# Kernel optimization log

Measured on AMD Instinct MI355X. Metric: run time of the kernel, lower is better.

## Reference

```python
import jax, jax.numpy as jnp
import numpy as np

NEG_INF = -jnp.inf


def setup_inputs() -> dict:
    key = jax.random.key(0)
    kq, kk, kv = jax.random.split(key, 3)
    B, L, H, E = 2, 2048, 16, 64
    queries = jax.random.normal(kq, (B, L, H, E), dtype=jnp.float32)
    keys = jax.random.normal(kk, (B, L, H, E), dtype=jnp.float32)
    values = jax.random.normal(kv, (B, L, H, E), dtype=jnp.float32)
    return {"queries": queries, "keys": keys, "values": values}


def reference(queries, keys, values):
    B, L, H, E = queries.shape
    scale = 1.0 / jnp.sqrt(jnp.asarray(E, dtype=queries.dtype))
    # scores: [B, H, L, S]
    scores = jnp.einsum("blhe,bshe->bhls", queries, keys)
    # causal mask: True above the diagonal -> masked out
    causal = jnp.triu(jnp.ones((L, L), dtype=bool), k=1)
    scores = jnp.where(causal[None, None, :, :], NEG_INF, scores)
    A = jax.nn.softmax(scale * scores, axis=-1)
    # output: [B, L, H, D]
    V = jnp.einsum("bhls,bshd->blhd", A, values)
    return V
```

## Files before the change

### kernel.cpp

```cpp
#include <hip/hip_runtime.h>


using f32x4  = __attribute__((ext_vector_type(4))) float;
using bf16x8 = __attribute__((ext_vector_type(8))) short;
using u32x2  = __attribute__((ext_vector_type(2))) unsigned int;
using u32x4  = __attribute__((ext_vector_type(4))) unsigned int;

constexpr int L = 2048;
constexpr int H = 16;
constexpr int E = 64;
constexpr int QBLK = 64;
constexpr int KVBLK = 64;
constexpr float QSC = 0.125f * 1.44269504088896f;
constexpr float THR = 8.0f;

__device__ __forceinline__ unsigned cvt_pk(float lo, float hi) {
    unsigned r;
    asm("v_cvt_pk_bf16_f32 %0, %1, %2" : "=v"(r) : "v"(lo), "v"(hi));
    return r;
}
__device__ __forceinline__ void pl16(unsigned& a, unsigned& b) {
    asm("v_permlane16_swap_b32 %0, %1" : "+v"(a), "+v"(b));
}
__device__ __forceinline__ void pl32(unsigned& a, unsigned& b) {
    asm("v_permlane32_swap_b32 %0, %1" : "+v"(a), "+v"(b));
}
__device__ __forceinline__ unsigned opaque_copy(unsigned a) {
    unsigned b;
    asm("v_mov_b32 %0, %1" : "=v"(b) : "v"(a));
    return b;
}
__device__ __forceinline__ float gmax4(float x) {
    unsigned a = __float_as_uint(x), b = opaque_copy(a);
    pl16(a, b);
    float m = fmaxf(__uint_as_float(a), __uint_as_float(b));
    unsigned c = __float_as_uint(m), d = opaque_copy(c);
    pl32(c, d);
    return fmaxf(__uint_as_float(c), __uint_as_float(d));
}
__device__ __forceinline__ float gsum4(float x) {
    unsigned a = __float_as_uint(x), b = opaque_copy(a);
    pl16(a, b);
    float s = __uint_as_float(a) + __uint_as_float(b);
    unsigned c = __float_as_uint(s), d = opaque_copy(c);
    pl32(c, d);
    return __uint_as_float(c) + __uint_as_float(d);
}
__device__ __forceinline__ int swz(int row, int bcol) {
    return (row * 128 + bcol) ^ ((row & 7) << 4);
}
__device__ __forceinline__ int swzV(int row, int bcol) {
    return (row * 128 + bcol) ^ ((((row & 7) ^ (row >> 3)) & 7) << 4);
}

__global__ __launch_bounds__(256, 4)
void fattn_kernel(const float* __restrict__ Q,
                  const float* __restrict__ K,
                  const float* __restrict__ V,
                  float* __restrict__ O)
{
    __shared__ short Kl[2][KVBLK * 64];
    __shared__ short Vl[2][64 * KVBLK];

    const int bx  = blockIdx.x;
    const int xcd = bx & 7;
    const int j   = bx >> 3;
    const int bh  = (j & 3) * 8 + xcd;
    const int v_  = j >> 2;
    const int q2  = v_ >> 3, x_ = v_ & 7;
    const int iq  = (q2 & 1) ? (31 - (q2 >> 1) - 2 * x_) : (2 * x_ + (q2 >> 1));
    const int h   = bh & 15;
    const int b   = bh >> 4;
    const int tid = threadIdx.x;
    const int w    = tid >> 6;
    const int lane = tid & 63;
    const int l16  = lane & 15;
    const int lhi  = lane >> 4;

    const size_t bhoff = (size_t)b * L * (H * E) + (size_t)h * E;
    const int rs_ = H * E;

    const int sv0 = (tid >> 4) * 4;
    const int d0  = (tid & 15) * 4;
    const int kc  = ((sv0 >> 3) & 1) * 32 + (sv0 >> 4) * 8 + (sv0 & 7);

    f32x4 ka[2][2];
    f32x4 va[4];

    auto issue_loads = [&](int t) {
        const int sb = t * KVBLK;
        #pragma unroll
        for (int g = 0; g < 2; ++g) {
            const int c = g * 256 + tid;
            const int s = c >> 3;
            const int e0 = (c & 7) * 8;
            const f32x4* kp = (const f32x4*)(K + bhoff + (size_t)(sb + s) * rs_ + e0);
            ka[g][0] = kp[0];
            ka[g][1] = kp[1];
        }
        #pragma unroll
        for (int jj = 0; jj < 4; ++jj)
            va[jj] = *(const f32x4*)(V + bhoff + (size_t)(sb + sv0 + jj) * rs_ + d0);
    };
    auto write_lds = [&](int bufi) {
        short* Kb = Kl[bufi];
        short* Vb = Vl[bufi];
        #pragma unroll
        for (int g = 0; g < 2; ++g) {
            const int c = g * 256 + tid;
            const int s = c >> 3;
            const int e0 = (c & 7) * 8;
            u32x4 kt;
            kt[0] = cvt_pk(ka[g][0][0], ka[g][0][1]);
            kt[1] = cvt_pk(ka[g][0][2], ka[g][0][3]);
            kt[2] = cvt_pk(ka[g][1][0], ka[g][1][1]);
            kt[3] = cvt_pk(ka[g][1][2], ka[g][1][3]);
            *(u32x4*)((char*)Kb + swz(s, e0 * 2)) = kt;
        }
        #pragma unroll
        for (int dd = 0; dd < 4; ++dd) {
            u32x2 vt;
            vt[0] = cvt_pk(va[0][dd], va[1][dd]);
            vt[1] = cvt_pk(va[2][dd], va[3][dd]);
            *(u32x2*)((char*)Vb + swzV(d0 + dd, kc * 2)) = vt;
        }
    };

    const int qg = iq * QBLK + w * 16 + l16;
    bf16x8 qf[2];
    {
        const float* qp = Q + bhoff + (size_t)qg * rs_ + lhi * 8;
        #pragma unroll
        for (int kf = 0; kf < 2; ++kf) {
            f32x4 xv = *(const f32x4*)(qp + kf * 32);
            f32x4 yv = *(const f32x4*)(qp + kf * 32 + 4);
            union { u32x4 u; bf16x8 hh; } r;
            r.u[0] = cvt_pk(xv[0] * QSC, xv[1] * QSC);
            r.u[1] = cvt_pk(xv[2] * QSC, xv[3] * QSC);
            r.u[2] = cvt_pk(yv[0] * QSC, yv[1] * QSC);
            r.u[3] = cvt_pk(yv[2] * QSC, yv[3] * QSC);
            qf[kf] = r.hh;
        }
    }

    float m_run = -INFINITY, lsum = 0.0f;
    f32x4 oacc[4];
    #pragma unroll
    for (int dt = 0; dt < 4; ++dt) oacc[dt] = (f32x4){0.f, 0.f, 0.f, 0.f};

    const int total = iq + 1;
    issue_loads(0);
    write_lds(0);
    if (total > 1) issue_loads(1);
    __syncthreads();

    for (int i = 0; i < total; ++i) {
        const char* Kb = (const char*)Kl[i & 1];
        const char* Vb = (const char*)Vl[i & 1];

        f32x4 p[4];
        #pragma unroll
        for (int st = 0; st < 4; ++st) p[st] = (f32x4){0.f, 0.f, 0.f, 0.f};
        __builtin_amdgcn_s_setprio(1);
        #pragma unroll
        for (int st = 0; st < 4; ++st) {
            #pragma unroll
            for (int kf = 0; kf < 2; ++kf) {
                bf16x8 af = *(const bf16x8*)(Kb + swz(st * 16 + l16, (lhi * 8 + kf * 32) * 2));
                p[st] = __builtin_amdgcn_mfma_f32_16x16x32_bf16(af, qf[kf], p[st], 0, 0, 0);
            }
        }
        __builtin_amdgcn_s_setprio(0);

        if (i == total - 1) {
            #pragma unroll
            for (int st = 0; st < 4; ++st)
                #pragma unroll
                for (int r = 0; r < 4; ++r) {
                    const int kg = i * KVBLK + st * 16 + lhi * 4 + r;
                    if (kg > qg) p[st][r] = -INFINITY;
                }
        }

        if (i + 1 < total) write_lds((i + 1) & 1);
        if (i + 2 < total) issue_loads(i + 2);

        float mx = -INFINITY;
        #pragma unroll
        for (int st = 0; st < 4; ++st)
            #pragma unroll
            for (int r = 0; r < 4; ++r) mx = fmaxf(mx, p[st][r]);
        mx = gmax4(mx);
        if (!__all(mx <= m_run + THR)) {
            const float mn = fmaxf(m_run, mx);
            const float corr = exp2f(m_run - mn);
            lsum *= corr;
            #pragma unroll
            for (int dt = 0; dt < 4; ++dt)
                #pragma unroll
                for (int r = 0; r < 4; ++r) oacc[dt][r] *= corr;
            m_run = mn;
        }
        float rsum = 0.f;
        #pragma unroll
        for (int st = 0; st < 4; ++st)
            #pragma unroll
            for (int r = 0; r < 4; ++r) {
                const float e = exp2f(p[st][r] - m_run);
                p[st][r] = e;
                rsum += e;
            }
        lsum += gsum4(rsum);

        unsigned wp[4][2];
        #pragma unroll
        for (int st = 0; st < 4; ++st) {
            wp[st][0] = cvt_pk(p[st][0], p[st][1]);
            wp[st][1] = cvt_pk(p[st][2], p[st][3]);
        }
        #pragma unroll
        for (int hh = 0; hh < 2; ++hh) {
            pl16(wp[0][hh], wp[1][hh]);
            pl16(wp[2][hh], wp[3][hh]);
            pl32(wp[0][hh], wp[2][hh]);
            pl32(wp[1][hh], wp[3][hh]);
        }
        union { u32x4 u; bf16x8 v; } pb0, pb1;
        pb0.u[0] = wp[0][0]; pb0.u[1] = wp[0][1];
        pb0.u[2] = wp[1][0]; pb0.u[3] = wp[1][1];
        pb1.u[0] = wp[2][0]; pb1.u[1] = wp[2][1];
        pb1.u[2] = wp[3][0]; pb1.u[3] = wp[3][1];

        __builtin_amdgcn_s_setprio(1);
        #pragma unroll
        for (int dt = 0; dt < 4; ++dt) {
            bf16x8 vf0 = *(const bf16x8*)(Vb + swzV(dt * 16 + l16, (lhi * 8) * 2));
            oacc[dt] = __builtin_amdgcn_mfma_f32_16x16x32_bf16(vf0, pb0.v, oacc[dt], 0, 0, 0);
            bf16x8 vf1 = *(const bf16x8*)(Vb + swzV(dt * 16 + l16, (lhi * 8 + 32) * 2));
            oacc[dt] = __builtin_amdgcn_mfma_f32_16x16x32_bf16(vf1, pb1.v, oacc[dt], 0, 0, 0);
        }
        __builtin_amdgcn_s_setprio(0);

        if (i + 1 < total) __syncthreads();
    }

    const float inv = 1.0f / lsum;
    float* op = O + bhoff + (size_t)qg * rs_;
    #pragma unroll
    for (int dt = 0; dt < 4; ++dt) {
        f32x4 o = oacc[dt];
        o[0] *= inv; o[1] *= inv; o[2] *= inv; o[3] *= inv;
        *(f32x4*)(op + dt * 16 + lhi * 4) = o;
    }
}

extern "C" void kernel_launch(void* const* d_in, const int* in_sizes, int n_in,
                              void* d_out, int out_size, void* d_ws, size_t ws_size,
                              hipStream_t stream) {
    const float* Q = (const float*)d_in[0];
    const float* K = (const float*)d_in[1];
    const float* V = (const float*)d_in[2];
    float* O = (float*)d_out;
    dim3 grid(1024);
    dim3 block(256);
    fattn_kernel<<<grid, block, 0, stream>>>(Q, K, V, O);
}
```

Baseline: 57.16 us.

## Pre-convert K/V to swizzled bf16 tiles in a prep kernel before attention

Adds a prep kernel that converts K and V to bf16 once, writing them into the workspace already in the swizzled LDS tile layout, with V transposed. The main attention kernel then copies these tiles straight from global memory into LDS, with no per-block fp32 loads, conversions or transposes. This removes the conversion work that every query block repeated for the same K/V tiles and halves the bytes each block reads. The cost is an extra kernel launch and a workspace round trip. The exp2 call is also switched to the hardware builtin, and the row max and row sum reductions are split into parallel chains.

Result: faster. 50.47 us (-11.7%).

```diff
diff --git a/kernel.cpp b/kernel.cpp
--- a/kernel.cpp
+++ b/kernel.cpp
@@ -14,6 +14,21 @@
 constexpr float QSC = 0.125f * 1.44269504088896f;
 constexpr float THR = 8.0f;
 
+#if defined(__has_builtin)
+#if __has_builtin(__builtin_amdgcn_exp2f)
+#define HAVE_EXP2 1
+#endif
+#endif
+__device__ __forceinline__ float fexp2(float x) {
+#ifdef HAVE_EXP2
+    return __builtin_amdgcn_exp2f(x);
+#else
+    float r;
+    asm("v_exp_f32 %0, %1" : "=v"(r) : "v"(x));
+    return r;
+#endif
+}
+
 __device__ __forceinline__ unsigned cvt_pk(float lo, float hi) {
     unsigned r;
     asm("v_cvt_pk_bf16_f32 %0, %1, %2" : "=v"(r) : "v"(lo), "v"(hi));
@@ -53,14 +68,64 @@
     return (row * 128 + bcol) ^ ((((row & 7) ^ (row >> 3)) & 7) << 4);
 }
 
+__global__ __launch_bounds__(256)
+void prep_kernel(const float* __restrict__ K, const float* __restrict__ V,
+                 short* __restrict__ Kb, short* __restrict__ Vb)
+{
+    __shared__ float Vt[64][65];
+    const int bx  = blockIdx.x;
+    const int t   = bx & 31;
+    const int bh  = bx >> 5;
+    const int tid = threadIdx.x;
+    const size_t bhoff = (size_t)(bh >> 4) * L * (H * E) + (size_t)(bh & 15) * E;
+    const size_t tileo = (size_t)(bh * 32 + t) * 4096;
+
+    #pragma unroll
+    for (int g = 0; g < 2; ++g) {
+        const int c  = g * 256 + tid;
+        const int r  = c >> 3;
+        const int e0 = (c & 7) * 8;
+        const float* kp = K + bhoff + (size_t)(t * 64 + r) * 1024 + e0;
+        f32x4 k0 = *(const f32x4*)kp, k1 = *(const f32x4*)(kp + 4);
+        u32x4 kt;
+        kt[0] = cvt_pk(k0[0], k0[1]); kt[1] = cvt_pk(k0[2], k0[3]);
+        kt[2] = cvt_pk(k1[0], k1[1]); kt[3] = cvt_pk(k1[2], k1[3]);
+        *(u32x4*)(Kb + tileo + r * 64 + (((e0 >> 3) ^ (r & 7)) * 8)) = kt;
+        const float* vp = V + bhoff + (size_t)(t * 64 + r) * 1024 + e0;
+        f32x4 v0 = *(const f32x4*)vp, v1 = *(const f32x4*)(vp + 4);
+        #pragma unroll
+        for (int k2 = 0; k2 < 4; ++k2) { Vt[r][e0 + k2] = v0[k2]; Vt[r][e0 + 4 + k2] = v1[k2]; }
+    }
+    __syncthreads();
+    #pragma unroll
+    for (int g = 0; g < 2; ++g) {
+        const int c  = g * 256 + tid;
+        const int d  = c >> 3;
+        const int jp = c & 7;
+        const int F  = ((d & 7) ^ (d >> 3)) & 7;
+        const int col0 = 8 * (jp ^ F);
+        float vals[8];
+        #pragma unroll
+        for (int i = 0; i < 8; ++i) {
+            const int col = col0 + i;
+            const int s = 16 * ((col >> 3) & 3) + 8 * (col >> 5) + (col & 7);
+            vals[i] = Vt[s][d];
+        }
+        u32x4 vt;
+        vt[0] = cvt_pk(vals[0], vals[1]); vt[1] = cvt_pk(vals[2], vals[3]);
+        vt[2] = cvt_pk(vals[4], vals[5]); vt[3] = cvt_pk(vals[6], vals[7]);
+        *(u32x4*)(Vb + tileo + d * 64 + jp * 8) = vt;
+    }
+}
+
 __global__ __launch_bounds__(256, 4)
-void fattn_kernel(const float* __restrict__ Q,
-                  const float* __restrict__ K,
-                  const float* __restrict__ V,
-                  float* __restrict__ O)
+void fattn_main(const float* __restrict__ Q,
+                const short* __restrict__ Kb,
+                const short* __restrict__ Vb,
+                float* __restrict__ O)
 {
-    __shared__ short Kl[2][KVBLK * 64];
-    __shared__ short Vl[2][64 * KVBLK];
+    __shared__ short Kl[2][4096];
+    __shared__ short Vl[2][4096];
 
     const int bx  = blockIdx.x;
     const int xcd = bx & 7;
@@ -69,24 +134,193 @@
     const int v_  = j >> 2;
     const int q2  = v_ >> 3, x_ = v_ & 7;
     const int iq  = (q2 & 1) ? (31 - (q2 >> 1) - 2 * x_) : (2 * x_ + (q2 >> 1));
-    const int h   = bh & 15;
-    const int b   = bh >> 4;
     const int tid = threadIdx.x;
     const int w    = tid >> 6;
     const int lane = tid & 63;
     const int l16  = lane & 15;
     const int lhi  = lane >> 4;
 
-    const size_t bhoff = (size_t)b * L * (H * E) + (size_t)h * E;
+    const size_t bhoff  = (size_t)(bh >> 4) * L * (H * E) + (size_t)(bh & 15) * E;
     const int rs_ = H * E;
-
+    const size_t kvbase = (size_t)bh * 32 * 4096;
+
+    u32x4 kreg[2], vreg[2];
+    auto stage_regs = [&](int t) {
+        const u32x4* kp = (const u32x4*)(Kb + kvbase + (size_t)t * 4096);
+        const u32x4* vp = (const u32x4*)(Vb + kvbase + (size_t)t * 4096);
+        #pragma unroll
+        for (int g = 0; g < 2; ++g) {
+            kreg[g] = kp[g * 256 + tid];
+            vreg[g] = vp[g * 256 + tid];
+        }
+    };
+    auto write_stage = [&](int buf) {
+        #pragma unroll
+        for (int g = 0; g < 2; ++g) {
+            ((u32x4*)Kl[buf])[g * 256 + tid] = kreg[g];
+            ((u32x4*)Vl[buf])[g * 256 + tid] = vreg[g];
+        }
+    };
+
+    const int qg = iq * QBLK + w * 16 + l16;
+    bf16x8 qf[2];
+    {
+        const float* qp = Q + bhoff + (size_t)qg * rs_ + lhi * 8;
+        #pragma unroll
+        for (int kf = 0; kf < 2; ++kf) {
+            f32x4 xv = *(const f32x4*)(qp + kf * 32);
+            f32x4 yv = *(const f32x4*)(qp + kf * 32 + 4);
+            union { u32x4 u; bf16x8 hh; } r;
+            r.u[0] = cvt_pk(xv[0] * QSC, xv[1] * QSC);
+            r.u[1] = cvt_pk(xv[2] * QSC, xv[3] * QSC);
+            r.u[2] = cvt_pk(yv[0] * QSC, yv[1] * QSC);
+            r.u[3] = cvt_pk(yv[2] * QSC, yv[3] * QSC);
+            qf[kf] = r.hh;
+        }
+    }
+
+    float m_run = -INFINITY, lsum = 0.0f;
+    f32x4 oacc[4];
+    #pragma unroll
+    for (int dt = 0; dt < 4; ++dt) oacc[dt] = (f32x4){0.f, 0.f, 0.f, 0.f};
+
+    const int total = iq + 1;
+    stage_regs(0);
+    write_stage(0);
+    if (total > 1) stage_regs(1);
+    __syncthreads();
+
+    for (int i = 0; i < total; ++i) {
+        const char* Kbl = (const char*)Kl[i & 1];
+        const char* Vbl = (const char*)Vl[i & 1];
+
+        f32x4 p[4];
+        #pragma unroll
+        for (int st = 0; st < 4; ++st) p[st] = (f32x4){0.f, 0.f, 0.f, 0.f};
+        __builtin_amdgcn_s_setprio(1);
+        #pragma unroll
+        for (int st = 0; st < 4; ++st) {
+            #pragma unroll
+            for (int kf = 0; kf < 2; ++kf) {
+                bf16x8 af = *(const bf16x8*)(Kbl + swz(st * 16 + l16, (lhi * 8 + kf * 32) * 2));
+                p[st] = __builtin_amdgcn_mfma_f32_16x16x32_bf16(af, qf[kf], p[st], 0, 0, 0);
+            }
+        }
+        __builtin_amdgcn_s_setprio(0);
+
+        if (i == total - 1) {
+            #pragma unroll
+            for (int st = 0; st < 4; ++st)
+                #pragma unroll
+                for (int r = 0; r < 4; ++r) {
+                    const int kg = i * KVBLK + st * 16 + lhi * 4 + r;
+                    if (kg > qg) p[st][r] = -INFINITY;
+                }
+        }
+
+        if (i + 1 < total) write_stage((i + 1) & 1);
+        if (i + 2 < total) stage_regs(i + 2);
+
+        f32x4 mv = p[0];
+        #pragma unroll
+        for (int st = 1; st < 4; ++st)
+            #pragma unroll
+            for (int r = 0; r < 4; ++r) mv[r] = fmaxf(mv[r], p[st][r]);
+        float mx = fmaxf(fmaxf(mv[0], mv[1]), fmaxf(mv[2], mv[3]));
+        mx = gmax4(mx);
+        if (!__all(mx <= m_run + THR)) {
+            const float mn = fmaxf(m_run, mx);
+            const float corr = fexp2(m_run - mn);
+            lsum *= corr;
+            #pragma unroll
+            for (int dt = 0; dt < 4; ++dt)
+                #pragma unroll
+                for (int r = 0; r < 4; ++r) oacc[dt][r] *= corr;
+            m_run = mn;
+        }
+        f32x4 rsv = (f32x4){0.f, 0.f, 0.f, 0.f};
+        #pragma unroll
+        for (int st = 0; st < 4; ++st)
+            #pragma unroll
+            for (int r = 0; r < 4; ++r) {
+                const float e = fexp2(p[st][r] - m_run);
+                p[st][r] = e;
+                rsv[r] += e;
+            }
+        lsum += gsum4((rsv[0] + rsv[1]) + (rsv[2] + rsv[3]));
+
+        unsigned wp[4][2];
+        #pragma unroll
+        for (int st = 0; st < 4; ++st) {
+            wp[st][0] = cvt_pk(p[st][0], p[st][1]);
+            wp[st][1] = cvt_pk(p[st][2], p[st][3]);
+        }
+        #pragma unroll
+        for (int hh = 0; hh < 2; ++hh) {
+            pl16(wp[0][hh], wp[1][hh]);
+            pl16(wp[2][hh], wp[3][hh]);
+            pl32(wp[0][hh], wp[2][hh]);
+            pl32(wp[1][hh], wp[3][hh]);
+        }
+        union { u32x4 u; bf16x8 v; } pb0, pb1;
+        pb0.u[0] = wp[0][0]; pb0.u[1] = wp[0][1];
+        pb0.u[2] = wp[1][0]; pb0.u[3] = wp[1][1];
+        pb1.u[0] = wp[2][0]; pb1.u[1] = wp[2][1];
+        pb1.u[2] = wp[3][0]; pb1.u[3] = wp[3][1];
+
+        __builtin_amdgcn_s_setprio(1);
+        #pragma unroll
+        for (int dt = 0; dt < 4; ++dt) {
+            bf16x8 vf0 = *(const bf16x8*)(Vbl + swzV(dt * 16 + l16, (lhi * 8) * 2));
+            oacc[dt] = __builtin_amdgcn_mfma_f32_16x16x32_bf16(vf0, pb0.v, oacc[dt], 0, 0, 0);
+            bf16x8 vf1 = *(const bf16x8*)(Vbl + swzV(dt * 16 + l16, (lhi * 8 + 32) * 2));
+            oacc[dt] = __builtin_amdgcn_mfma_f32_16x16x32_bf16(vf1, pb1.v, oacc[dt], 0, 0, 0);
+        }
+        __builtin_amdgcn_s_setprio(0);
+
+        if (i + 1 < total) __syncthreads();
+    }
+
+    const float inv = 1.0f / lsum;
+    float* op = O + bhoff + (size_t)qg * rs_;
+    #pragma unroll
+    for (int dt = 0; dt < 4; ++dt) {
+        f32x4 o = oacc[dt];
+        o[0] *= inv; o[1] *= inv; o[2] *= inv; o[3] *= inv;
+        *(f32x4*)(op + dt * 16 + lhi * 4) = o;
+    }
+}
+
+__global__ __launch_bounds__(256, 4)
+void fattn_fb(const float* __restrict__ Q,
+              const float* __restrict__ K,
+              const float* __restrict__ V,
+              float* __restrict__ O)
+{
+    __shared__ short Kl[2][KVBLK * 64];
+    __shared__ short Vl[2][64 * KVBLK];
+
+    const int bx  = blockIdx.x;
+    const int xcd = bx & 7;
+    const int j   = bx >> 3;
+    const int bh  = (j & 3) * 8 + xcd;
+    const int v_  = j >> 2;
+    const int q2  = v_ >> 3, x_ = v_ & 7;
+    const int iq  = (q2 & 1) ? (31 - (q2 >> 1) - 2 * x_) : (2 * x_ + (q2 >> 1));
+    const int tid = threadIdx.x;
+    const int w    = tid >> 6;
+    const int lane = tid & 63;
+    const int l16  = lane & 15;
+    const int lhi  = lane >> 4;
+
+    const size_t bhoff = (size_t)(bh >> 4) * L * (H * E) + (size_t)(bh & 15) * E;
+    const int rs_ = H * E;
     const int sv0 = (tid >> 4) * 4;
     const int d0  = (tid & 15) * 4;
     const int kc  = ((sv0 >> 3) & 1) * 32 + (sv0 >> 4) * 8 + (sv0 & 7);
 
     f32x4 ka[2][2];
     f32x4 va[4];
-
     auto issue_loads = [&](int t) {
         const int sb = t * KVBLK;
         #pragma unroll
@@ -155,9 +389,8 @@
     __syncthreads();
 
     for (int i = 0; i < total; ++i) {
-        const char* Kb = (const char*)Kl[i & 1];
-        const char* Vb = (const char*)Vl[i & 1];
-
+        const char* Kbl = (const char*)Kl[i & 1];
+        const char* Vbl = (const char*)Vl[i & 1];
         f32x4 p[4];
         #pragma unroll
         for (int st = 0; st < 4; ++st) p[st] = (f32x4){0.f, 0.f, 0.f, 0.f};
@@ -166,12 +399,11 @@
         for (int st = 0; st < 4; ++st) {
             #pragma unroll
             for (int kf = 0; kf < 2; ++kf) {
-                bf16x8 af = *(const bf16x8*)(Kb + swz(st * 16 + l16, (lhi * 8 + kf * 32) * 2));
+                bf16x8 af = *(const bf16x8*)(Kbl + swz(st * 16 + l16, (lhi * 8 + kf * 32) * 2));
                 p[st] = __builtin_amdgcn_mfma_f32_16x16x32_bf16(af, qf[kf], p[st], 0, 0, 0);
             }
         }
         __builtin_amdgcn_s_setprio(0);
-
         if (i == total - 1) {
             #pragma unroll
             for (int st = 0; st < 4; ++st)
@@ -181,19 +413,19 @@
                     if (kg > qg) p[st][r] = -INFINITY;
                 }
         }
-
         if (i + 1 < total) write_lds((i + 1) & 1);
         if (i + 2 < total) issue_loads(i + 2);
 
-        float mx = -INFINITY;
-        #pragma unroll
-        for (int st = 0; st < 4; ++st)
-            #pragma unroll
-            for (int r = 0; r < 4; ++r) mx = fmaxf(mx, p[st][r]);
+        f32x4 mv = p[0];
+        #pragma unroll
+        for (int st = 1; st < 4; ++st)
+            #pragma unroll
+            for (int r = 0; r < 4; ++r) mv[r] = fmaxf(mv[r], p[st][r]);
+        float mx = fmaxf(fmaxf(mv[0], mv[1]), fmaxf(mv[2], mv[3]));
         mx = gmax4(mx);
         if (!__all(mx <= m_run + THR)) {
             const float mn = fmaxf(m_run, mx);
-            const float corr = exp2f(m_run - mn);
+            const float corr = fexp2(m_run - mn);
             lsum *= corr;
             #pragma unroll
             for (int dt = 0; dt < 4; ++dt)
@@ -201,16 +433,16 @@
                 for (int r = 0; r < 4; ++r) oacc[dt][r] *= corr;
             m_run = mn;
         }
-        float rsum = 0.f;
+        f32x4 rsv = (f32x4){0.f, 0.f, 0.f, 0.f};
         #pragma unroll
         for (int st = 0; st < 4; ++st)
             #pragma unroll
             for (int r = 0; r < 4; ++r) {
-                const float e = exp2f(p[st][r] - m_run);
+                const float e = fexp2(p[st][r] - m_run);
                 p[st][r] = e;
-                rsum += e;
+                rsv[r] += e;
             }
-        lsum += gsum4(rsum);
+        lsum += gsum4((rsv[0] + rsv[1]) + (rsv[2] + rsv[3]));
 
         unsigned wp[4][2];
         #pragma unroll
@@ -234,13 +466,12 @@
         __builtin_amdgcn_s_setprio(1);
         #pragma unroll
         for (int dt = 0; dt < 4; ++dt) {
-            bf16x8 vf0 = *(const bf16x8*)(Vb + swzV(dt * 16 + l16, (lhi * 8) * 2));
+            bf16x8 vf0 = *(const bf16x8*)(Vbl + swzV(dt * 16 + l16, (lhi * 8) * 2));
             oacc[dt] = __builtin_amdgcn_mfma_f32_16x16x32_bf16(vf0, pb0.v, oacc[dt], 0, 0, 0);
-            bf16x8 vf1 = *(const bf16x8*)(Vb + swzV(dt * 16 + l16, (lhi * 8 + 32) * 2));
+            bf16x8 vf1 = *(const bf16x8*)(Vbl + swzV(dt * 16 + l16, (lhi * 8 + 32) * 2));
             oacc[dt] = __builtin_amdgcn_mfma_f32_16x16x32_bf16(vf1, pb1.v, oacc[dt], 0, 0, 0);
         }
         __builtin_amdgcn_s_setprio(0);
-
         if (i + 1 < total) __syncthreads();
     }
 
@@ -261,7 +492,13 @@
     const float* K = (const float*)d_in[1];
     const float* V = (const float*)d_in[2];
     float* O = (float*)d_out;
-    dim3 grid(1024);
-    dim3 block(256);
-    fattn_kernel<<<grid, block, 0, stream>>>(Q, K, V, O);
-}
+    const size_t kb_elems = (size_t)32 * 32 * 4096;
+    if (ws_size >= 2 * kb_elems * sizeof(short)) {
+        short* Kb = (short*)d_ws;
+        short* Vb = Kb + kb_elems;
+        prep_kernel<<<1024, 256, 0, stream>>>(K, V, Kb, Vb);
+        fattn_main<<<1024, 256, 0, stream>>>(Q, Kb, Vb, O);
+    } else {
+        fattn_fb<<<1024, 256, 0, stream>>>(Q, K, V, O);
+    }
+}
```
